# Kernel tuning notes

Measured on AMD Instinct MI355X. Metric: run time of the kernel, lower is better.

Reference implementation:

```python
import jax, jax.numpy as jnp
import numpy as np

D_K = 64  # module-level constant in source
NEG = -1e9


def setup_inputs() -> dict:
    key = jax.random.key(0)
    k1, k2, k3, k4 = jax.random.split(key, 4)
    B, H, S, D = 4, 16, 2048, 64
    query = jax.random.normal(k1, (B, H, S, D), dtype=jnp.float32)
    key_t = jax.random.normal(k2, (B, H, S, D), dtype=jnp.float32)
    value = jax.random.normal(k3, (B, H, S, D), dtype=jnp.float32)
    mask = jax.random.randint(k4, (B, 1, S, S), 0, 2) == 1  # bool, broadcast over heads
    return {"query": query, "key": key_t, "value": value, "mask": mask}


def reference(query, key, value, mask):
    # scores = QK^T / sqrt(d_k)   [B,H,S,S]
    scores = jnp.einsum("bhqd,bhkd->bhqk", query, key) / jnp.sqrt(jnp.float32(D_K))
    # masked_fill_(mask, -1e9)
    scores = jnp.where(mask, jnp.float32(NEG), scores)
    # non-standard: multiply masked scores by V, then log_softmax over last dim
    out = jnp.einsum("bhqk,bhkd->bhqd", scores, value)  # [B,H,S,d_v]
    return jax.nn.log_softmax(out, axis=-1)
```

## Files before the change

### kernel.cpp

```cpp
#include <hip/hip_runtime.h>
#include <hip/hip_bf16.h>


typedef __attribute__((ext_vector_type(8))) short bf16x8;
typedef __attribute__((ext_vector_type(16))) float f32x16;

#define NEGV (-1e9f)
#define NEGBITS 0xCE6E6B28u

__device__ inline unsigned cvt_bf16(float f) {
    unsigned u = __builtin_bit_cast(unsigned, f);
    u += 0x7FFFu + ((u >> 16) & 1u);
    return u >> 16;
}
__device__ inline unsigned pk_bf16(float a, float b) {
    return cvt_bf16(a) | (cvt_bf16(b) << 16);
}
__device__ inline unsigned pk_trunc(float a, float b) {
    return __builtin_amdgcn_perm(__builtin_bit_cast(unsigned, b),
                                 __builtin_bit_cast(unsigned, a), 0x07060302u);
}

#define WS_KV_OFF  2097152u
#define WS_NEED    39845888ull

__global__ __launch_bounds__(256)
void preconv(const int* __restrict__ M, const float* __restrict__ K,
             const float* __restrict__ V, unsigned long long* __restrict__ bitT,
             unsigned short* __restrict__ KV) {
    const int tid  = threadIdx.x;
    const int lane = tid & 63;
    const int bid  = blockIdx.x;

    if (bid < 2048) {
        const int gw = (bid * 256 + tid) >> 6;
        const int b  = gw >> 11;
        const int qt = (gw >> 8) & 7;
        const int q  = gw & 255;
        const size_t mbase = (size_t)gw * 2048;
        unsigned long long* dst = bitT + (size_t)(b * 8 + qt) * 32 * 256 + q;
#pragma unroll 4
        for (int ki = 0; ki < 32; ki++) {
            const int m = M[mbase + ki * 64 + lane];
            const unsigned long long bal = __ballot(m != 0);
            if (lane == 0) dst[ki * 256] = bal;
        }
    } else if (bid < 6144) {
        const unsigned g   = (unsigned)(bid - 2048) * 256 + tid;
        const int c        = g & 7;
        const unsigned rid = g >> 3;
        const int r        = rid & 63;
        const unsigned tile = rid >> 6;
        const float* src = K + (size_t)rid * 64 + c * 8;
        const float4 f0 = *(const float4*)(src);
        const float4 f1 = *(const float4*)(src + 4);
        uint4 p;
        p.x = pk_trunc(f0.x, f0.y); p.y = pk_trunc(f0.z, f0.w);
        p.z = pk_trunc(f1.x, f1.y); p.w = pk_trunc(f1.z, f1.w);
        *(uint4*)&KV[(size_t)tile * 9216 + r * 72 + c * 8] = p;
    } else {
        const unsigned g = (unsigned)(bid - 6144) * 256 + tid;
        const int d  = g & 63;
        const int c  = (g >> 6) & 7;
        const int ki = (g >> 9) & 31;
        const int bh = g >> 14;
        const float* src = V + ((size_t)(bh * 2048 + ki * 64 + c * 8) * 64 + d);
        float v[8];
#pragma unroll
        for (int j = 0; j < 8; j++) v[j] = src[j * 64];
        uint4 p;
        p.x = pk_trunc(v[0], v[1]); p.y = pk_trunc(v[2], v[3]);
        p.z = pk_trunc(v[4], v[5]); p.w = pk_trunc(v[6], v[7]);
        *(uint4*)&KV[(size_t)(bh * 32 + ki) * 9216 + 4608 + d * 72 + c * 8] = p;
    }
}

__global__ __launch_bounds__(256, 4)
void attn_fast(const float* __restrict__ Q,
               const unsigned short* __restrict__ KV,
               const unsigned long long* __restrict__ bitT,
               float* __restrict__ Out) {
    __shared__ __attribute__((aligned(16))) unsigned short sT[2][9216];

    const int tid  = threadIdx.x;
    const int wave = tid >> 6;
    const int lane = tid & 63;
    const int half = lane >> 5;
    const int l32  = lane & 31;

    const int bid = blockIdx.x;
    const int h   = bid & 15;
    const int qt2 = (bid >> 4) & 15;
    const int b   = bid >> 8;
    const int bh  = b * 16 + h;
    const int q0  = qt2 * 128;
    const int qt  = qt2 >> 1;
    const int qh  = qt2 & 1;

    const float* Qb = Q + (size_t)(bh * 2048 + q0) * 64;
    const unsigned short* Tg = KV + (size_t)bh * 32 * 9216;
    const unsigned long long* Bt = bitT + (size_t)(b * 8 + qt) * 32 * 256
                                 + qh * 128 + wave * 32 + l32;

    #define STAGE(buf, ki) do {                                                   \
        const unsigned short* g_ = Tg + (size_t)(ki) * 9216;                      \
        unsigned short* l_ = sT[buf];                                             \
        _Pragma("unroll")                                                         \
        for (int q_ = 0; q_ < 4; q_++)                                            \
            __builtin_amdgcn_global_load_lds(                                     \
                (const __attribute__((address_space(1))) void*)                   \
                    (g_ + q_ * 2048 + wave * 512 + lane * 8),                     \
                (__attribute__((address_space(3))) void*)                         \
                    (l_ + q_ * 2048 + wave * 512), 16, 0, 0);                     \
        _Pragma("unroll")                                                         \
        for (int s_ = 0; s_ < 2; s_++)                                            \
            __builtin_amdgcn_global_load_lds(                                     \
                (const __attribute__((address_space(1))) void*)                   \
                    (g_ + 8192 + s_ * 512 + wave * 128 + lane * 2),               \
                (__attribute__((address_space(3))) void*)                         \
                    (l_ + 8192 + s_ * 512 + wave * 128), 4, 0, 0);                \
    } while (0)

    STAGE(0, 0);
    unsigned long long mw = Bt[0];

    bf16x8 qF[4];
    {
        const float* qr = Qb + (size_t)(wave * 32 + l32) * 64 + half * 8;
#pragma unroll
        for (int dk = 0; dk < 4; dk++) {
            const float4 f0 = *(const float4*)(qr + dk * 16);
            const float4 f1 = *(const float4*)(qr + dk * 16 + 4);
            union { bf16x8 v; unsigned u[4]; } t;
            t.u[0] = pk_bf16(f0.x * 0.125f, f0.y * 0.125f);
            t.u[1] = pk_bf16(f0.z * 0.125f, f0.w * 0.125f);
            t.u[2] = pk_bf16(f1.x * 0.125f, f1.y * 0.125f);
            t.u[3] = pk_bf16(f1.z * 0.125f, f1.w * 0.125f);
            qF[dk] = t.v;
        }
    }

    f32x16 Oacc[2];
#pragma unroll
    for (int db = 0; db < 2; db++)
#pragma unroll
        for (int r = 0; r < 16; r++) Oacc[db][r] = 0.f;

    __syncthreads();

    for (int ki = 0; ki < 32; ki++) {
        const int cur = ki & 1;

        unsigned long long mwN = 0;
        if (ki < 31) {
            STAGE(cur ^ 1, ki + 1);
            mwN = Bt[(ki + 1) * 256];
        }

#pragma unroll
        for (int jk = 0; jk < 2; jk++) {
            bf16x8 aK[4];
#pragma unroll
            for (int dk = 0; dk < 4; dk++)
                aK[dk] = *(const bf16x8*)&sT[cur][(jk * 32 + l32) * 72 + dk * 16 + half * 8];
            bf16x8 bV[2][2];
#pragma unroll
            for (int p = 0; p < 2; p++)
#pragma unroll
                for (int db = 0; db < 2; db++)
                    bV[p][db] = *(const bf16x8*)&sT[cur][4608 + (db * 32 + l32) * 72
                                                         + (jk * 2 + p) * 16 + half * 8];

            const unsigned b32 = (unsigned)(mw >> (jk * 32));
            const unsigned bsh = b32 >> (half * 4);

            f32x16 acc;
#pragma unroll
            for (int rg = 0; rg < 4; rg++) {
#pragma unroll
                for (int w = 0; w < 4; w++) {
                    const int pos = rg * 8 + w;
                    const int sb = ((int)(bsh << (31 - pos))) >> 31;
                    acc[rg * 4 + w] = __builtin_bit_cast(float, (unsigned)sb & NEGBITS);
                }
            }
#pragma unroll
            for (int dk = 0; dk < 4; dk++)
                acc = __builtin_amdgcn_mfma_f32_32x32x16_bf16(aK[dk], qF[dk], acc, 0, 0, 0);

#pragma unroll
            for (int p = 0; p < 2; p++) {
                const unsigned P0 = pk_trunc(acc[p * 8 + 0], acc[p * 8 + 1]);
                const unsigned P1 = pk_trunc(acc[p * 8 + 2], acc[p * 8 + 3]);
                const unsigned P2 = pk_trunc(acc[p * 8 + 4], acc[p * 8 + 5]);
                const unsigned P3 = pk_trunc(acc[p * 8 + 6], acc[p * 8 + 7]);
                auto r02 = __builtin_amdgcn_permlane32_swap(P0, P2, false, false);
                auto r13 = __builtin_amdgcn_permlane32_swap(P1, P3, false, false);
                union { bf16x8 v; unsigned u[4]; } aS;
                aS.u[0] = (unsigned)r02[0];
                aS.u[1] = (unsigned)r13[0];
                aS.u[2] = (unsigned)r02[1];
                aS.u[3] = (unsigned)r13[1];
#pragma unroll
                for (int db = 0; db < 2; db++)
                    Oacc[db] = __builtin_amdgcn_mfma_f32_32x32x16_bf16(aS.v, bV[p][db], Oacc[db], 0, 0, 0);
            }
        }

        mw = mwN;
        __syncthreads();
    }

    float* Ob = Out + (size_t)bh * 2048 * 64;
#pragma unroll
    for (int r = 0; r < 16; r++) {
        const float v0 = Oacc[0][r], v1 = Oacc[1][r];
        float mx = fmaxf(v0, v1);
#pragma unroll
        for (int off = 1; off < 32; off <<= 1)
            mx = fmaxf(mx, __shfl_xor(mx, off, 64));
        float s = __expf(v0 - mx) + __expf(v1 - mx);
#pragma unroll
        for (int off = 1; off < 32; off <<= 1)
            s += __shfl_xor(s, off, 64);
        const float lse = mx + __logf(s);
        const int qrow = q0 + wave * 32 + (r & 3) + 8 * (r >> 2) + 4 * half;
        Ob[(size_t)qrow * 64 + l32]      = v0 - lse;
        Ob[(size_t)qrow * 64 + 32 + l32] = v1 - lse;
    }
    #undef STAGE
}

__global__ __launch_bounds__(256)
void mask_pack(const int* __restrict__ M, unsigned long long* __restrict__ bitT) {
    const int lane = threadIdx.x & 63;
    const int gw   = (blockIdx.x * 256 + threadIdx.x) >> 6;
    const int b    = gw >> 11;
    const int qt   = (gw >> 8) & 7;
    const int q    = gw & 255;
    const size_t mbase = (size_t)gw * 2048;
    unsigned long long* dst = bitT + (size_t)(b * 8 + qt) * 32 * 256 + q;
#pragma unroll 4
    for (int ki = 0; ki < 32; ki++) {
        const int m = M[mbase + ki * 64 + lane];
        const unsigned long long bal = __ballot(m != 0);
        if (lane == 0) dst[ki * 256] = bal;
    }
}

__global__ __launch_bounds__(256, 4)
void attn_v10(const float* __restrict__ Q, const float* __restrict__ K,
              const float* __restrict__ V,
              const unsigned long long* __restrict__ bitT,
              float* __restrict__ Out) {
    __shared__ __attribute__((aligned(16))) unsigned short sK[2][64 * 72];
    __shared__ __attribute__((aligned(16))) unsigned short sVt[2][64 * 72];

    const int tid  = threadIdx.x;
    const int wave = tid >> 6;
    const int lane = tid & 63;
    const int half = lane >> 5;
    const int l32  = lane & 31;

    const int bid = blockIdx.x;
    const int h   = bid & 15;
    const int qt2 = (bid >> 4) & 15;
    const int b   = bid >> 8;
    const int bh  = b * 16 + h;
    const int q0  = qt2 * 128;
    const int qt  = qt2 >> 1;
    const int qh  = qt2 & 1;

    const float* Qb = Q + (size_t)(bh * 2048 + q0) * 64;
    const float* Kb = K + (size_t)bh * 2048 * 64;
    const float* Vb = V + (size_t)bh * 2048 * 64;
    const unsigned long long* Bt = bitT + (size_t)(b * 8 + qt) * 32 * 256
                                 + qh * 128 + wave * 32 + l32;

    float4 kp[4];
    float  vp[16];
    unsigned long long mw = Bt[0];
    const int krow = tid >> 4, kc4 = tid & 15;
#pragma unroll
    for (int i = 0; i < 4; i++)
        kp[i] = *(const float4*)(Kb + (size_t)(krow + i * 16) * 64 + kc4 * 4);
#pragma unroll
    for (int i = 0; i < 2; i++) {
        const int kb = (wave * 2 + i) * 8;
#pragma unroll
        for (int j = 0; j < 8; j++)
            vp[i * 8 + j] = Vb[(size_t)(kb + j) * 64 + lane];
    }

    bf16x8 qF[4];
    {
        const float* qr = Qb + (size_t)(wave * 32 + l32) * 64 + half * 8;
#pragma unroll
        for (int dk = 0; dk < 4; dk++) {
            const float4 f0 = *(const float4*)(qr + dk * 16);
            const float4 f1 = *(const float4*)(qr + dk * 16 + 4);
            union { bf16x8 v; unsigned u[4]; } t;
            t.u[0] = pk_bf16(f0.x * 0.125f, f0.y * 0.125f);
            t.u[1] = pk_bf16(f0.z * 0.125f, f0.w * 0.125f);
            t.u[2] = pk_bf16(f1.x * 0.125f, f1.y * 0.125f);
            t.u[3] = pk_bf16(f1.z * 0.125f, f1.w * 0.125f);
            qF[dk] = t.v;
        }
    }

    f32x16 Oacc[2];
#pragma unroll
    for (int db = 0; db < 2; db++)
#pragma unroll
        for (int r = 0; r < 16; r++) Oacc[db][r] = 0.f;

    for (int ki = 0; ki < 32; ki++) {
        const int cur = ki & 1;
#pragma unroll
        for (int i = 0; i < 4; i++) {
            uint2 p;
            p.x = pk_trunc(kp[i].x, kp[i].y);
            p.y = pk_trunc(kp[i].z, kp[i].w);
            *(uint2*)&sK[cur][(krow + i * 16) * 72 + kc4 * 4] = p;
        }
#pragma unroll
        for (int i = 0; i < 2; i++) {
            const int kb = (wave * 2 + i) * 8;
            uint4 p4;
            p4.x = pk_trunc(vp[i * 8 + 0], vp[i * 8 + 1]);
            p4.y = pk_trunc(vp[i * 8 + 2], vp[i * 8 + 3]);
            p4.z = pk_trunc(vp[i * 8 + 4], vp[i * 8 + 5]);
            p4.w = pk_trunc(vp[i * 8 + 6], vp[i * 8 + 7]);
            *(uint4*)&sVt[cur][lane * 72 + kb] = p4;
        }

        __syncthreads();

        unsigned long long mwN = 0;
        if (ki < 31) {
            const int kn = (ki + 1) * 64;
            mwN = Bt[(ki + 1) * 256];
#pragma unroll
            for (int i = 0; i < 4; i++)
                kp[i] = *(const float4*)(Kb + (size_t)(kn + krow + i * 16) * 64 + kc4 * 4);
#pragma unroll
            for (int i = 0; i < 2; i++) {
                const int kb = (wave * 2 + i) * 8;
#pragma unroll
                for (int j = 0; j < 8; j++)
                    vp[i * 8 + j] = Vb[(size_t)(kn + kb + j) * 64 + lane];
            }
        }

#pragma unroll
        for (int jk = 0; jk < 2; jk++) {
            bf16x8 aK[4];
#pragma unroll
            for (int dk = 0; dk < 4; dk++)
                aK[dk] = *(const bf16x8*)&sK[cur][(jk * 32 + l32) * 72 + dk * 16 + half * 8];
            bf16x8 bV[2][2];
#pragma unroll
            for (int p = 0; p < 2; p++)
#pragma unroll
                for (int db = 0; db < 2; db++)
                    bV[p][db] = *(const bf16x8*)&sVt[cur][(db * 32 + l32) * 72 + (jk * 2 + p) * 16 + half * 8];

            const unsigned b32 = (unsigned)(mw >> (jk * 32));
            const unsigned bsh = b32 >> (half * 4);

            f32x16 acc;
#pragma unroll
            for (int rg = 0; rg < 4; rg++) {
                const unsigned nib = bsh >> (rg * 8);
                acc[rg * 4 + 0] = (nib & 1u) ? NEGV : 0.f;
                acc[rg * 4 + 1] = (nib & 2u) ? NEGV : 0.f;
                acc[rg * 4 + 2] = (nib & 4u) ? NEGV : 0.f;
                acc[rg * 4 + 3] = (nib & 8u) ? NEGV : 0.f;
            }
#pragma unroll
            for (int dk = 0; dk < 4; dk++)
                acc = __builtin_amdgcn_mfma_f32_32x32x16_bf16(aK[dk], qF[dk], acc, 0, 0, 0);

#pragma unroll
            for (int p = 0; p < 2; p++) {
                const unsigned P0 = pk_trunc(acc[p * 8 + 0], acc[p * 8 + 1]);
                const unsigned P1 = pk_trunc(acc[p * 8 + 2], acc[p * 8 + 3]);
                const unsigned P2 = pk_trunc(acc[p * 8 + 4], acc[p * 8 + 5]);
                const unsigned P3 = pk_trunc(acc[p * 8 + 6], acc[p * 8 + 7]);
                auto r02 = __builtin_amdgcn_permlane32_swap(P0, P2, false, false);
                auto r13 = __builtin_amdgcn_permlane32_swap(P1, P3, false, false);
                union { bf16x8 v; unsigned u[4]; } aS;
                aS.u[0] = (unsigned)r02[0];
                aS.u[1] = (unsigned)r13[0];
                aS.u[2] = (unsigned)r02[1];
                aS.u[3] = (unsigned)r13[1];
#pragma unroll
                for (int db = 0; db < 2; db++)
                    Oacc[db] = __builtin_amdgcn_mfma_f32_32x32x16_bf16(aS.v, bV[p][db], Oacc[db], 0, 0, 0);
            }
        }

        mw = mwN;
    }

    float* Ob = Out + (size_t)bh * 2048 * 64;
#pragma unroll
    for (int r = 0; r < 16; r++) {
        const float v0 = Oacc[0][r], v1 = Oacc[1][r];
        float mx = fmaxf(v0, v1);
#pragma unroll
        for (int off = 1; off < 32; off <<= 1)
            mx = fmaxf(mx, __shfl_xor(mx, off, 64));
        float s = __expf(v0 - mx) + __expf(v1 - mx);
#pragma unroll
        for (int off = 1; off < 32; off <<= 1)
            s += __shfl_xor(s, off, 64);
        const float lse = mx + __logf(s);
        const int qrow = q0 + wave * 32 + (r & 3) + 8 * (r >> 2) + 4 * half;
        Ob[(size_t)qrow * 64 + l32]      = v0 - lse;
        Ob[(size_t)qrow * 64 + 32 + l32] = v1 - lse;
    }
}

extern "C" void kernel_launch(void* const* d_in, const int* in_sizes, int n_in,
                              void* d_out, int out_size, void* d_ws, size_t ws_size,
                              hipStream_t stream) {
    const float* Q = (const float*)d_in[0];
    const float* K = (const float*)d_in[1];
    const float* V = (const float*)d_in[2];
    const int*   M = (const int*)d_in[3];
    float* Out = (float*)d_out;
    unsigned long long* bitT = (unsigned long long*)d_ws;

    if (ws_size >= WS_NEED) {
        unsigned short* KV = (unsigned short*)((char*)d_ws + WS_KV_OFF);
        preconv<<<dim3(10240), dim3(256), 0, stream>>>(M, K, V, bitT, KV);
        attn_fast<<<dim3(1024), dim3(256), 0, stream>>>(Q, KV, bitT, Out);
    } else {
        mask_pack<<<dim3(2048), dim3(256), 0, stream>>>(M, bitT);
        attn_v10<<<dim3(1024), dim3(256), 0, stream>>>(Q, K, V, bitT, Out);
    }
}
```

Before: 276.6 us.

## Pre-swizzle K/V into MFMA fragment order and load directly from global

The preconv kernel now stages each 64x64 K and V tile through shared memory and writes bf16 data in exact per-lane MFMA fragment order, with V transposed. The attention kernel drops its LDS double-buffer, its global_load_lds staging and its per-iteration barriers. Each lane instead reads its fragments straight from global memory as contiguous 16-byte loads. This removes LDS traffic and synchronisation, but each of the 16 q-blocks per head now reads K/V from L2 with no prefetch to hide latency.

```diff
diff --git a/kernel.cpp b/kernel.cpp
--- a/kernel.cpp
+++ b/kernel.cpp
@@ -21,8 +21,8 @@
                                  __builtin_bit_cast(unsigned, a), 0x07060302u);
 }
 
-#define WS_KV_OFF  2097152u
-#define WS_NEED    39845888ull
+#define WS_KV_OFF 2097152u
+#define WS_NEED   (2097152ull + 2048ull * 16384ull)
 
 __global__ __launch_bounds__(256)
 void preconv(const int* __restrict__ M, const float* __restrict__ K,
@@ -45,33 +45,56 @@
             const unsigned long long bal = __ballot(m != 0);
             if (lane == 0) dst[ki * 256] = bal;
         }
-    } else if (bid < 6144) {
-        const unsigned g   = (unsigned)(bid - 2048) * 256 + tid;
-        const int c        = g & 7;
-        const unsigned rid = g >> 3;
-        const int r        = rid & 63;
-        const unsigned tile = rid >> 6;
-        const float* src = K + (size_t)rid * 64 + c * 8;
-        const float4 f0 = *(const float4*)(src);
-        const float4 f1 = *(const float4*)(src + 4);
+        return;
+    }
+
+    __shared__ float sF[64][68];
+    const int tile = bid - 2048;
+    const float* Ksrc = K + (size_t)tile * 64 * 64;
+    const float* Vsrc = V + (size_t)tile * 64 * 64;
+    unsigned short* KF = KV + (size_t)tile * 8192;
+    unsigned short* VF = KF + 4096;
+
+#pragma unroll
+    for (int k = 0; k < 4; k++) {
+        const int f = tid + k * 256;
+        const int row = f >> 4, c4 = f & 15;
+        *(float4*)&sF[row][c4 * 4] = *(const float4*)(Ksrc + row * 64 + c4 * 4);
+    }
+    __syncthreads();
+#pragma unroll
+    for (int k = 0; k < 2; k++) {
+        const int kc = tid + k * 256;
+        const int jk = kc >> 8, dk = (kc >> 6) & 3, ln = kc & 63;
+        const int r  = jk * 32 + (ln & 31);
+        const int e0 = dk * 16 + (ln >> 5) * 8;
+        const float* s = &sF[r][e0];
         uint4 p;
-        p.x = pk_trunc(f0.x, f0.y); p.y = pk_trunc(f0.z, f0.w);
-        p.z = pk_trunc(f1.x, f1.y); p.w = pk_trunc(f1.z, f1.w);
-        *(uint4*)&KV[(size_t)tile * 9216 + r * 72 + c * 8] = p;
-    } else {
-        const unsigned g = (unsigned)(bid - 6144) * 256 + tid;
-        const int d  = g & 63;
-        const int c  = (g >> 6) & 7;
-        const int ki = (g >> 9) & 31;
-        const int bh = g >> 14;
-        const float* src = V + ((size_t)(bh * 2048 + ki * 64 + c * 8) * 64 + d);
+        p.x = pk_trunc(s[0], s[1]); p.y = pk_trunc(s[2], s[3]);
+        p.z = pk_trunc(s[4], s[5]); p.w = pk_trunc(s[6], s[7]);
+        *(uint4*)&KF[kc * 8] = p;
+    }
+    __syncthreads();
+#pragma unroll
+    for (int k = 0; k < 4; k++) {
+        const int f = tid + k * 256;
+        const int row = f >> 4, c4 = f & 15;
+        *(float4*)&sF[row][c4 * 4] = *(const float4*)(Vsrc + row * 64 + c4 * 4);
+    }
+    __syncthreads();
+#pragma unroll
+    for (int k = 0; k < 2; k++) {
+        const int vc  = tid + k * 256;
+        const int jk2 = vc >> 7, db = (vc >> 6) & 1, ln = vc & 63;
+        const int d   = db * 32 + (ln & 31);
+        const int kk0 = jk2 * 16 + (ln >> 5) * 8;
         float v[8];
 #pragma unroll
-        for (int j = 0; j < 8; j++) v[j] = src[j * 64];
+        for (int j = 0; j < 8; j++) v[j] = sF[kk0 + j][d];
         uint4 p;
         p.x = pk_trunc(v[0], v[1]); p.y = pk_trunc(v[2], v[3]);
         p.z = pk_trunc(v[4], v[5]); p.w = pk_trunc(v[6], v[7]);
-        *(uint4*)&KV[(size_t)(bh * 32 + ki) * 9216 + 4608 + d * 72 + c * 8] = p;
+        *(uint4*)&VF[vc * 8] = p;
     }
 }
 
@@ -80,8 +103,6 @@
                const unsigned short* __restrict__ KV,
                const unsigned long long* __restrict__ bitT,
                float* __restrict__ Out) {
-    __shared__ __attribute__((aligned(16))) unsigned short sT[2][9216];
-
     const int tid  = threadIdx.x;
     const int wave = tid >> 6;
     const int lane = tid & 63;
@@ -98,31 +119,9 @@
     const int qh  = qt2 & 1;
 
     const float* Qb = Q + (size_t)(bh * 2048 + q0) * 64;
-    const unsigned short* Tg = KV + (size_t)bh * 32 * 9216;
+    const unsigned short* Tg = KV + (size_t)bh * 32 * 8192;
     const unsigned long long* Bt = bitT + (size_t)(b * 8 + qt) * 32 * 256
                                  + qh * 128 + wave * 32 + l32;
-
-    #define STAGE(buf, ki) do {                                                   \
-        const unsigned short* g_ = Tg + (size_t)(ki) * 9216;                      \
-        unsigned short* l_ = sT[buf];                                             \
-        _Pragma("unroll")                                                         \
-        for (int q_ = 0; q_ < 4; q_++)                                            \
-            __builtin_amdgcn_global_load_lds(                                     \
-                (const __attribute__((address_space(1))) void*)                   \
-                    (g_ + q_ * 2048 + wave * 512 + lane * 8),                     \
-                (__attribute__((address_space(3))) void*)                         \
-                    (l_ + q_ * 2048 + wave * 512), 16, 0, 0);                     \
-        _Pragma("unroll")                                                         \
-        for (int s_ = 0; s_ < 2; s_++)                                            \
-            __builtin_amdgcn_global_load_lds(                                     \
-                (const __attribute__((address_space(1))) void*)                   \
-                    (g_ + 8192 + s_ * 512 + wave * 128 + lane * 2),               \
-                (__attribute__((address_space(3))) void*)                         \
-                    (l_ + 8192 + s_ * 512 + wave * 128), 4, 0, 0);                \
-    } while (0)
-
-    STAGE(0, 0);
-    unsigned long long mw = Bt[0];
 
     bf16x8 qF[4];
     {
@@ -146,30 +145,25 @@
 #pragma unroll
         for (int r = 0; r < 16; r++) Oacc[db][r] = 0.f;
 
-    __syncthreads();
+    unsigned long long mw = Bt[0];
 
     for (int ki = 0; ki < 32; ki++) {
-        const int cur = ki & 1;
-
-        unsigned long long mwN = 0;
-        if (ki < 31) {
-            STAGE(cur ^ 1, ki + 1);
-            mwN = Bt[(ki + 1) * 256];
-        }
+        const unsigned short* T = Tg + ki * 8192;
+        const unsigned long long mwN = (ki < 31) ? Bt[(ki + 1) * 256] : 0ull;
 
 #pragma unroll
         for (int jk = 0; jk < 2; jk++) {
             bf16x8 aK[4];
 #pragma unroll
             for (int dk = 0; dk < 4; dk++)
-                aK[dk] = *(const bf16x8*)&sT[cur][(jk * 32 + l32) * 72 + dk * 16 + half * 8];
+                aK[dk] = *(const bf16x8*)(T + ((jk * 4 + dk) * 64 + lane) * 8);
             bf16x8 bV[2][2];
 #pragma unroll
             for (int p = 0; p < 2; p++)
 #pragma unroll
                 for (int db = 0; db < 2; db++)
-                    bV[p][db] = *(const bf16x8*)&sT[cur][4608 + (db * 32 + l32) * 72
-                                                         + (jk * 2 + p) * 16 + half * 8];
+                    bV[p][db] = *(const bf16x8*)(T + 4096 +
+                        (((jk * 2 + p) * 2 + db) * 64 + lane) * 8);
 
             const unsigned b32 = (unsigned)(mw >> (jk * 32));
             const unsigned bsh = b32 >> (half * 4);
@@ -208,7 +202,6 @@
         }
 
         mw = mwN;
-        __syncthreads();
     }
 
     float* Ob = Out + (size_t)bh * 2048 * 64;
@@ -228,7 +221,6 @@
         Ob[(size_t)qrow * 64 + l32]      = v0 - lse;
         Ob[(size_t)qrow * 64 + 32 + l32] = v1 - lse;
     }
-    #undef STAGE
 }
 
 __global__ __launch_bounds__(256)
@@ -434,7 +426,7 @@
 
     if (ws_size >= WS_NEED) {
         unsigned short* KV = (unsigned short*)((char*)d_ws + WS_KV_OFF);
-        preconv<<<dim3(10240), dim3(256), 0, stream>>>(M, K, V, bitT, KV);
+        preconv<<<dim3(4096), dim3(256), 0, stream>>>(M, K, V, bitT, KV);
         attn_fast<<<dim3(1024), dim3(256), 0, stream>>>(Q, KV, bitT, Out);
     } else {
         mask_pack<<<dim3(2048), dim3(256), 0, stream>>>(M, bitT);
```

Result: faster. 268.1 us (-3.1%).
